# Kernel tuning notes

Hardware: AMD Instinct MI355X
Metric: run time of the kernel (lower is better)

## Reference

```python
import jax, jax.numpy as jnp
import numpy as np

TEMPERATURE = 1.0
B, H, S, D = 2, 16, 2048, 128

def setup_inputs() -> dict:
    key = jax.random.key(0)
    kq, kk, kv = jax.random.split(key, 3)
    q = jax.random.normal(kq, (B, H, S, D), dtype=jnp.float32)
    k = jax.random.normal(kk, (B, H, S, D), dtype=jnp.float32)
    v = jax.random.normal(kv, (B, H, S, D), dtype=jnp.float32)
    alpha = jnp.float32(0.5)  # nn.Parameter(torch.tensor(0.5))
    return {"q": q, "k": k, "v": v, "alpha": alpha}

def reference(q, k, v, alpha):
    # scores: [B,H,S,S]
    scores = jnp.einsum('bhqd,bhkd->bhqk', q, k) / TEMPERATURE
    row_mean = jnp.mean(scores, axis=-1, keepdims=True)  # [B,H,S,1]
    adaptive = alpha * scores + (1.0 - alpha) * row_mean
    attn = jax.nn.softmax(adaptive, axis=-1)
    return jnp.einsum('bhqk,bhkd->bhqd', attn, v)
```

## Files before the change

### kernel.cpp

```cpp
#include <hip/hip_runtime.h>


#define S_LEN 2048
#define HD    128
#define BQ    128
#define BK    64
#define NW    4
#define NT    (S_LEN / BK)
#define TILE_USH 16384

typedef __bf16    bf16x8 __attribute__((ext_vector_type(8)));
typedef __bf16    bf16x4 __attribute__((ext_vector_type(4)));
typedef _Float16  f16x8  __attribute__((ext_vector_type(8)));
typedef float     f32x4  __attribute__((ext_vector_type(4)));

__device__ __forceinline__ unsigned short f2bf(float x) {
  unsigned u = __builtin_bit_cast(unsigned, x);
  u = (u + 0x7FFFu + ((u >> 16) & 1u)) >> 16;
  return (unsigned short)u;
}
__device__ __forceinline__ unsigned short f2h(float x) {
  _Float16 h = (_Float16)x;
  return __builtin_bit_cast(unsigned short, h);
}
__device__ __forceinline__ float fast_exp2(float x) {
#if __has_builtin(__builtin_amdgcn_exp2f)
  return __builtin_amdgcn_exp2f(x);
#else
  return exp2f(x);
#endif
}

__global__ __launch_bounds__(256) void attn_prepass_kernel(
    const float* __restrict__ kg, const float* __restrict__ vg,
    unsigned short* __restrict__ ws) {
  const int blk  = blockIdx.x;
  const int head = blk >> 5;
  const int kt   = blk & 31;
  const int tid  = threadIdx.x;
  const size_t hoff = (size_t)head * S_LEN * HD;
  const float* kp = kg + hoff + (size_t)kt * BK * HD;
  const float* vp = vg + hoff + (size_t)kt * BK * HD;
  unsigned short* wsK  = ws + (size_t)blk * TILE_USH;
  unsigned short* wsVt = wsK + 8192;

#pragma unroll
  for (int it = 0; it < 4; ++it) {
    int idx = it * 256 + tid;
    int key = idx >> 4;
    int ch  = idx & 15;
    const float* src = kp + key * HD + ch * 8;
    float4 a = *(const float4*)src;
    float4 b = *(const float4*)(src + 4);
    float xs[8] = {a.x, a.y, a.z, a.w, b.x, b.y, b.z, b.w};
    union { unsigned short s[8]; uint4 v; } hi;
#pragma unroll
    for (int j = 0; j < 8; ++j) hi.s[j] = f2h(xs[j]);
    int slot = (ch & 8) | ((ch & 7) ^ (key & 7));
    *(uint4*)&wsK[key * 128 + slot * 8] = hi.v;
  }

#pragma unroll
  for (int it = 0; it < 4; ++it) {
    int idx = it * 256 + tid;
    int ch  = idx >> 7;
    int dim = idx & 127;
    union { unsigned short s[8]; uint4 v; } g;
#pragma unroll
    for (int j = 0; j < 8; ++j)
      g.s[j] = f2bf(vp[(size_t)(ch * 8 + j) * HD + dim]);
    int slot = ch ^ (dim & 7);
    *(uint4*)&wsVt[dim * 64 + slot * 8] = g.v;
  }
}

__device__ __forceinline__ void stage_tile(const unsigned short* __restrict__ wt,
                                           unsigned short* dst, int tid, int w) {
#pragma unroll
  for (int r = 0; r < 8; ++r) {
    const unsigned int* gp = (const unsigned int*)(wt + (size_t)(r * 256 + tid) * 8);
    unsigned short* lp = dst + (size_t)(r * 256 + w * 64) * 8;
    __builtin_amdgcn_global_load_lds(
        (const __attribute__((address_space(1))) unsigned int*)gp,
        (__attribute__((address_space(3))) unsigned int*)lp, 16, 0, 0);
  }
}

__global__ __launch_bounds__(256, 2) void adaptive_attn_kernel(
    const float* __restrict__ qg, const unsigned short* __restrict__ ws,
    const float* __restrict__ alphap, float* __restrict__ out) {
  __shared__ unsigned short sBuf[2][TILE_USH];
  __shared__ unsigned short sP[NW][2][1024];

  const int b    = blockIdx.x;
  const int head = (b & 7) * 4 + ((b >> 3) & 3);
  const int qt   = b >> 5;

  const int tid  = threadIdx.x;
  const int w    = tid >> 6;
  const int lane = tid & 63;
  const int g    = lane >> 4;
  const int qi   = lane & 15;

  const float lscale = alphap[0] * 1.44269504088896f;

  f16x8 qf[2][4];
#pragma unroll
  for (int h = 0; h < 2; ++h) {
    const int qrow = qt * BQ + w * 32 + h * 16 + qi;
    const float* qp = qg + (size_t)head * S_LEN * HD + (size_t)qrow * HD;
#pragma unroll
    for (int c = 0; c < 4; ++c) {
      float4 a  = *(const float4*)(qp + c * 32 + g * 8);
      float4 bb = *(const float4*)(qp + c * 32 + g * 8 + 4);
      float xs[8] = {a.x, a.y, a.z, a.w, bb.x, bb.y, bb.z, bb.w};
      union { f16x8 v; _Float16 s[8]; } hh;
#pragma unroll
      for (int j = 0; j < 8; ++j) hh.s[j] = (_Float16)(xs[j] * lscale);
      qf[h][c] = hh.v;
    }
  }

  f32x4 o[2][8];
#pragma unroll
  for (int h = 0; h < 2; ++h)
#pragma unroll
    for (int dt = 0; dt < 8; ++dt) o[h][dt] = (f32x4){0.f, 0.f, 0.f, 0.f};
  float lrun[2] = {0.f, 0.f};

  const unsigned short* wsh = ws + (size_t)head * NT * TILE_USH;

  stage_tile(wsh, &sBuf[0][0], tid, w);
  __syncthreads();

  for (int kt = 0; kt < NT; ++kt) {
    const unsigned short* sK  = &sBuf[kt & 1][0];
    const unsigned short* sVt = sK + 8192;

    if (kt + 1 < NT)
      stage_tile(wsh + (size_t)(kt + 1) * TILE_USH, &sBuf[(kt + 1) & 1][0], tid, w);

    f32x4 st[2][4];
#pragma unroll
    for (int mt = 0; mt < 4; ++mt) {
      f32x4 a0 = (f32x4){0.f, 0.f, 0.f, 0.f};
      f32x4 a1 = (f32x4){0.f, 0.f, 0.f, 0.f};
#pragma unroll
      for (int c = 0; c < 4; ++c) {
        int ch   = c * 4 + g;
        int slot = (ch & 8) | ((ch & 7) ^ (qi & 7));
        f16x8 ah = *(const f16x8*)&sK[(mt * 16 + qi) * 128 + slot * 8];
        a0 = __builtin_amdgcn_mfma_f32_16x16x32_f16(ah, qf[0][c], a0, 0, 0, 0);
        a1 = __builtin_amdgcn_mfma_f32_16x16x32_f16(ah, qf[1][c], a1, 0, 0, 0);
      }
      st[0][mt] = a0; st[1][mt] = a1;
    }

#pragma unroll
    for (int h = 0; h < 2; ++h) {
      unsigned short* sPh = &sP[w][h][0];
#pragma unroll
      for (int mt = 0; mt < 4; ++mt) {
        float p0 = fast_exp2(st[h][mt][0]);
        float p1 = fast_exp2(st[h][mt][1]);
        float p2 = fast_exp2(st[h][mt][2]);
        float p3 = fast_exp2(st[h][mt][3]);
        lrun[h] += (p0 + p1) + (p2 + p3);
        bf16x4 pv4;
        pv4[0] = (__bf16)p0; pv4[1] = (__bf16)p1;
        pv4[2] = (__bf16)p2; pv4[3] = (__bf16)p3;
        int slot = (mt * 2 + (g >> 1)) ^ (qi & 7);
        *(bf16x4*)&sPh[qi * 64 + slot * 8 + (g & 1) * 4] = pv4;
      }
    }

    bf16x8 pf[2][2];
#pragma unroll
    for (int h = 0; h < 2; ++h)
#pragma unroll
      for (int c = 0; c < 2; ++c) {
        int slot = (c * 4 + g) ^ (qi & 7);
        pf[h][c] = *(const bf16x8*)&sP[w][h][qi * 64 + slot * 8];
      }

#pragma unroll
    for (int dt = 0; dt < 8; ++dt) {
      f32x4 a0 = o[0][dt];
      f32x4 a1 = o[1][dt];
#pragma unroll
      for (int c = 0; c < 2; ++c) {
        int slot = (c * 4 + g) ^ (qi & 7);
        bf16x8 vf = *(const bf16x8*)&sVt[(dt * 16 + qi) * 64 + slot * 8];
        a0 = __builtin_amdgcn_mfma_f32_16x16x32_bf16(pf[0][c], vf, a0, 0, 0, 0);
        a1 = __builtin_amdgcn_mfma_f32_16x16x32_bf16(pf[1][c], vf, a1, 0, 0, 0);
      }
      o[0][dt] = a0; o[1][dt] = a1;
    }

    __syncthreads();
  }

  float* oph = out + (size_t)head * S_LEN * HD + (size_t)(qt * BQ + w * 32) * HD;
#pragma unroll
  for (int h = 0; h < 2; ++h) {
    float ltot = lrun[h];
    ltot += __shfl_xor(ltot, 16, 64);
    ltot += __shfl_xor(ltot, 32, 64);
    float inv[4];
#pragma unroll
    for (int r = 0; r < 4; ++r) {
      float lr = __shfl(ltot, g * 4 + r, 64);
      inv[r] = 1.0f / lr;
    }
    float* op = oph + (size_t)(h * 16) * HD;
#pragma unroll
    for (int dt = 0; dt < 8; ++dt) {
#pragma unroll
      for (int r = 0; r < 4; ++r) {
        op[(size_t)(g * 4 + r) * HD + dt * 16 + qi] = o[h][dt][r] * inv[r];
      }
    }
  }
}

extern "C" void kernel_launch(void* const* d_in, const int* in_sizes, int n_in,
                              void* d_out, int out_size, void* d_ws, size_t ws_size,
                              hipStream_t stream) {
  const float* q     = (const float*)d_in[0];
  const float* k     = (const float*)d_in[1];
  const float* v     = (const float*)d_in[2];
  const float* alpha = (const float*)d_in[3];
  float* out = (float*)d_out;
  unsigned short* ws = (unsigned short*)d_ws;

  hipLaunchKernelGGL(attn_prepass_kernel, dim3(1024), dim3(256), 0, stream,
                     k, v, ws);
  hipLaunchKernelGGL(adaptive_attn_kernel, dim3(512), dim3(256), 0, stream,
                     q, ws, alpha, out);
}
```

Before: 201.4 us.

## Software-pipeline PV MFMA one tile behind and transpose V via LDS

```diff
diff --git a/kernel.cpp b/kernel.cpp
--- a/kernel.cpp
+++ b/kernel.cpp
@@ -34,6 +34,7 @@
 __global__ __launch_bounds__(256) void attn_prepass_kernel(
     const float* __restrict__ kg, const float* __restrict__ vg,
     unsigned short* __restrict__ ws) {
+  __shared__ float T[64 * 130];
   const int blk  = blockIdx.x;
   const int head = blk >> 5;
   const int kt   = blk & 31;
@@ -61,16 +62,25 @@
   }
 
 #pragma unroll
-  for (int it = 0; it < 4; ++it) {
+  for (int it = 0; it < 16; ++it) {
     int idx = it * 256 + tid;
-    int ch  = idx >> 7;
-    int dim = idx & 127;
-    union { unsigned short s[8]; uint4 v; } g;
-#pragma unroll
-    for (int j = 0; j < 8; ++j)
-      g.s[j] = f2bf(vp[(size_t)(ch * 8 + j) * HD + dim]);
+    int key = idx >> 6;
+    int c2  = idx & 63;
+    float2 a = *(const float2*)(vp + (size_t)key * HD + c2 * 2);
+    *(float2*)&T[key * 130 + c2 * 2] = a;
+  }
+  __syncthreads();
+
+#pragma unroll
+  for (int r = 0; r < 4; ++r) {
+    int idx = r * 256 + tid;
+    int dim = idx >> 3;
+    int ch  = idx & 7;
+    union { unsigned short s[8]; uint4 v; } gg;
+#pragma unroll
+    for (int j = 0; j < 8; ++j) gg.s[j] = f2bf(T[(ch * 8 + j) * 130 + dim]);
     int slot = ch ^ (dim & 7);
-    *(uint4*)&wsVt[dim * 64 + slot * 8] = g.v;
+    *(uint4*)&wsVt[dim * 64 + slot * 8] = gg.v;
   }
 }
 
@@ -128,6 +138,9 @@
     for (int dt = 0; dt < 8; ++dt) o[h][dt] = (f32x4){0.f, 0.f, 0.f, 0.f};
   float lrun[2] = {0.f, 0.f};
 
+  bf16x8 vreg[8][2];
+  bf16x8 pf[2][2];
+
   const unsigned short* wsh = ws + (size_t)head * NT * TILE_USH;
 
   stage_tile(wsh, &sBuf[0][0], tid, w);
@@ -141,6 +154,7 @@
       stage_tile(wsh + (size_t)(kt + 1) * TILE_USH, &sBuf[(kt + 1) & 1][0], tid, w);
 
     f32x4 st[2][4];
+    __builtin_amdgcn_s_setprio(1);
 #pragma unroll
     for (int mt = 0; mt < 4; ++mt) {
       f32x4 a0 = (f32x4){0.f, 0.f, 0.f, 0.f};
@@ -154,6 +168,23 @@
         a1 = __builtin_amdgcn_mfma_f32_16x16x32_f16(ah, qf[1][c], a1, 0, 0, 0);
       }
       st[0][mt] = a0; st[1][mt] = a1;
+    }
+    __builtin_amdgcn_s_setprio(0);
+
+    if (kt > 0) {
+      __builtin_amdgcn_s_setprio(1);
+#pragma unroll
+      for (int dt = 0; dt < 8; ++dt) {
+        f32x4 a0 = o[0][dt];
+        f32x4 a1 = o[1][dt];
+#pragma unroll
+        for (int c = 0; c < 2; ++c) {
+          a0 = __builtin_amdgcn_mfma_f32_16x16x32_bf16(pf[0][c], vreg[dt][c], a0, 0, 0, 0);
+          a1 = __builtin_amdgcn_mfma_f32_16x16x32_bf16(pf[1][c], vreg[dt][c], a1, 0, 0, 0);
+        }
+        o[0][dt] = a0; o[1][dt] = a1;
+      }
+      __builtin_amdgcn_s_setprio(0);
     }
 
 #pragma unroll
@@ -174,7 +205,6 @@
       }
     }
 
-    bf16x8 pf[2][2];
 #pragma unroll
     for (int h = 0; h < 2; ++h)
 #pragma unroll
@@ -184,21 +214,29 @@
       }
 
 #pragma unroll
-    for (int dt = 0; dt < 8; ++dt) {
-      f32x4 a0 = o[0][dt];
-      f32x4 a1 = o[1][dt];
+    for (int dt = 0; dt < 8; ++dt)
 #pragma unroll
       for (int c = 0; c < 2; ++c) {
         int slot = (c * 4 + g) ^ (qi & 7);
-        bf16x8 vf = *(const bf16x8*)&sVt[(dt * 16 + qi) * 64 + slot * 8];
-        a0 = __builtin_amdgcn_mfma_f32_16x16x32_bf16(pf[0][c], vf, a0, 0, 0, 0);
-        a1 = __builtin_amdgcn_mfma_f32_16x16x32_bf16(pf[1][c], vf, a1, 0, 0, 0);
-      }
-      o[0][dt] = a0; o[1][dt] = a1;
-    }
+        vreg[dt][c] = *(const bf16x8*)&sVt[(dt * 16 + qi) * 64 + slot * 8];
+      }
 
     __syncthreads();
   }
+
+  __builtin_amdgcn_s_setprio(1);
+#pragma unroll
+  for (int dt = 0; dt < 8; ++dt) {
+    f32x4 a0 = o[0][dt];
+    f32x4 a1 = o[1][dt];
+#pragma unroll
+    for (int c = 0; c < 2; ++c) {
+      a0 = __builtin_amdgcn_mfma_f32_16x16x32_bf16(pf[0][c], vreg[dt][c], a0, 0, 0, 0);
+      a1 = __builtin_amdgcn_mfma_f32_16x16x32_bf16(pf[1][c], vreg[dt][c], a1, 0, 0, 0);
+    }
+    o[0][dt] = a0; o[1][dt] = a1;
+  }
+  __builtin_amdgcn_s_setprio(0);
 
   float* oph = out + (size_t)head * S_LEN * HD + (size_t)(qt * BQ + w * 32) * HD;
 #pragma unroll
```

Result: no change. 200.8 us (-0.3%).

## Use two waves with 64 query rows each and transpose V via LDS

Applied to the files above, without the earlier changes.

```diff
diff --git a/kernel.cpp b/kernel.cpp
--- a/kernel.cpp
+++ b/kernel.cpp
@@ -5,7 +5,8 @@
 #define HD    128
 #define BQ    128
 #define BK    64
-#define NW    4
+#define NW    2
+#define NH    4
 #define NT    (S_LEN / BK)
 #define TILE_USH 16384
 
@@ -34,6 +35,7 @@
 __global__ __launch_bounds__(256) void attn_prepass_kernel(
     const float* __restrict__ kg, const float* __restrict__ vg,
     unsigned short* __restrict__ ws) {
+  __shared__ float T[64 * 130];
   const int blk  = blockIdx.x;
   const int head = blk >> 5;
   const int kt   = blk & 31;
@@ -61,36 +63,45 @@
   }
 
 #pragma unroll
-  for (int it = 0; it < 4; ++it) {
+  for (int it = 0; it < 16; ++it) {
     int idx = it * 256 + tid;
-    int ch  = idx >> 7;
-    int dim = idx & 127;
-    union { unsigned short s[8]; uint4 v; } g;
-#pragma unroll
-    for (int j = 0; j < 8; ++j)
-      g.s[j] = f2bf(vp[(size_t)(ch * 8 + j) * HD + dim]);
+    int key = idx >> 6;
+    int c2  = idx & 63;
+    float2 a = *(const float2*)(vp + (size_t)key * HD + c2 * 2);
+    *(float2*)&T[key * 130 + c2 * 2] = a;
+  }
+  __syncthreads();
+
+#pragma unroll
+  for (int r = 0; r < 4; ++r) {
+    int idx = r * 256 + tid;
+    int dim = idx >> 3;
+    int ch  = idx & 7;
+    union { unsigned short s[8]; uint4 v; } gg;
+#pragma unroll
+    for (int j = 0; j < 8; ++j) gg.s[j] = f2bf(T[(ch * 8 + j) * 130 + dim]);
     int slot = ch ^ (dim & 7);
-    *(uint4*)&wsVt[dim * 64 + slot * 8] = g.v;
+    *(uint4*)&wsVt[dim * 64 + slot * 8] = gg.v;
   }
 }
 
 __device__ __forceinline__ void stage_tile(const unsigned short* __restrict__ wt,
                                            unsigned short* dst, int tid, int w) {
 #pragma unroll
-  for (int r = 0; r < 8; ++r) {
-    const unsigned int* gp = (const unsigned int*)(wt + (size_t)(r * 256 + tid) * 8);
-    unsigned short* lp = dst + (size_t)(r * 256 + w * 64) * 8;
+  for (int r = 0; r < 16; ++r) {
+    const unsigned int* gp = (const unsigned int*)(wt + (size_t)(r * 128 + tid) * 8);
+    unsigned short* lp = dst + (size_t)(r * 128 + w * 64) * 8;
     __builtin_amdgcn_global_load_lds(
         (const __attribute__((address_space(1))) unsigned int*)gp,
         (__attribute__((address_space(3))) unsigned int*)lp, 16, 0, 0);
   }
 }
 
-__global__ __launch_bounds__(256, 2) void adaptive_attn_kernel(
+__global__ __launch_bounds__(128, 1) void adaptive_attn_kernel(
     const float* __restrict__ qg, const unsigned short* __restrict__ ws,
     const float* __restrict__ alphap, float* __restrict__ out) {
   __shared__ unsigned short sBuf[2][TILE_USH];
-  __shared__ unsigned short sP[NW][2][1024];
+  __shared__ unsigned short sP[NW][NH][1024];
 
   const int b    = blockIdx.x;
   const int head = (b & 7) * 4 + ((b >> 3) & 3);
@@ -104,10 +115,10 @@
 
   const float lscale = alphap[0] * 1.44269504088896f;
 
-  f16x8 qf[2][4];
-#pragma unroll
-  for (int h = 0; h < 2; ++h) {
-    const int qrow = qt * BQ + w * 32 + h * 16 + qi;
+  f16x8 qf[NH][4];
+#pragma unroll
+  for (int h = 0; h < NH; ++h) {
+    const int qrow = qt * BQ + w * 64 + h * 16 + qi;
     const float* qp = qg + (size_t)head * S_LEN * HD + (size_t)qrow * HD;
 #pragma unroll
     for (int c = 0; c < 4; ++c) {
@@ -121,12 +132,12 @@
     }
   }
 
-  f32x4 o[2][8];
-#pragma unroll
-  for (int h = 0; h < 2; ++h)
+  f32x4 o[NH][8];
+#pragma unroll
+  for (int h = 0; h < NH; ++h)
 #pragma unroll
     for (int dt = 0; dt < 8; ++dt) o[h][dt] = (f32x4){0.f, 0.f, 0.f, 0.f};
-  float lrun[2] = {0.f, 0.f};
+  float lrun[NH] = {0.f, 0.f, 0.f, 0.f};
 
   const unsigned short* wsh = ws + (size_t)head * NT * TILE_USH;
 
@@ -140,43 +151,39 @@
     if (kt + 1 < NT)
       stage_tile(wsh + (size_t)(kt + 1) * TILE_USH, &sBuf[(kt + 1) & 1][0], tid, w);
 
-    f32x4 st[2][4];
 #pragma unroll
     for (int mt = 0; mt < 4; ++mt) {
-      f32x4 a0 = (f32x4){0.f, 0.f, 0.f, 0.f};
-      f32x4 a1 = (f32x4){0.f, 0.f, 0.f, 0.f};
+      f32x4 acc[NH];
+#pragma unroll
+      for (int h = 0; h < NH; ++h) acc[h] = (f32x4){0.f, 0.f, 0.f, 0.f};
 #pragma unroll
       for (int c = 0; c < 4; ++c) {
         int ch   = c * 4 + g;
         int slot = (ch & 8) | ((ch & 7) ^ (qi & 7));
         f16x8 ah = *(const f16x8*)&sK[(mt * 16 + qi) * 128 + slot * 8];
-        a0 = __builtin_amdgcn_mfma_f32_16x16x32_f16(ah, qf[0][c], a0, 0, 0, 0);
-        a1 = __builtin_amdgcn_mfma_f32_16x16x32_f16(ah, qf[1][c], a1, 0, 0, 0);
-      }
-      st[0][mt] = a0; st[1][mt] = a1;
-    }
-
-#pragma unroll
-    for (int h = 0; h < 2; ++h) {
-      unsigned short* sPh = &sP[w][h][0];
-#pragma unroll
-      for (int mt = 0; mt < 4; ++mt) {
-        float p0 = fast_exp2(st[h][mt][0]);
-        float p1 = fast_exp2(st[h][mt][1]);
-        float p2 = fast_exp2(st[h][mt][2]);
-        float p3 = fast_exp2(st[h][mt][3]);
+        acc[0] = __builtin_amdgcn_mfma_f32_16x16x32_f16(ah, qf[0][c], acc[0], 0, 0, 0);
+        acc[1] = __builtin_amdgcn_mfma_f32_16x16x32_f16(ah, qf[1][c], acc[1], 0, 0, 0);
+        acc[2] = __builtin_amdgcn_mfma_f32_16x16x32_f16(ah, qf[2][c], acc[2], 0, 0, 0);
+        acc[3] = __builtin_amdgcn_mfma_f32_16x16x32_f16(ah, qf[3][c], acc[3], 0, 0, 0);
+      }
+#pragma unroll
+      for (int h = 0; h < NH; ++h) {
+        float p0 = fast_exp2(acc[h][0]);
+        float p1 = fast_exp2(acc[h][1]);
+        float p2 = fast_exp2(acc[h][2]);
+        float p3 = fast_exp2(acc[h][3]);
         lrun[h] += (p0 + p1) + (p2 + p3);
         bf16x4 pv4;
         pv4[0] = (__bf16)p0; pv4[1] = (__bf16)p1;
         pv4[2] = (__bf16)p2; pv4[3] = (__bf16)p3;
         int slot = (mt * 2 + (g >> 1)) ^ (qi & 7);
-        *(bf16x4*)&sPh[qi * 64 + slot * 8 + (g & 1) * 4] = pv4;
-      }
-    }
-
-    bf16x8 pf[2][2];
-#pragma unroll
-    for (int h = 0; h < 2; ++h)
+        *(bf16x4*)&sP[w][h][qi * 64 + slot * 8 + (g & 1) * 4] = pv4;
+      }
+    }
+
+    bf16x8 pf[NH][2];
+#pragma unroll
+    for (int h = 0; h < NH; ++h)
 #pragma unroll
       for (int c = 0; c < 2; ++c) {
         int slot = (c * 4 + g) ^ (qi & 7);
@@ -185,24 +192,23 @@
 
 #pragma unroll
     for (int dt = 0; dt < 8; ++dt) {
-      f32x4 a0 = o[0][dt];
-      f32x4 a1 = o[1][dt];
 #pragma unroll
       for (int c = 0; c < 2; ++c) {
         int slot = (c * 4 + g) ^ (qi & 7);
         bf16x8 vf = *(const bf16x8*)&sVt[(dt * 16 + qi) * 64 + slot * 8];
-        a0 = __builtin_amdgcn_mfma_f32_16x16x32_bf16(pf[0][c], vf, a0, 0, 0, 0);
-        a1 = __builtin_amdgcn_mfma_f32_16x16x32_bf16(pf[1][c], vf, a1, 0, 0, 0);
-      }
-      o[0][dt] = a0; o[1][dt] = a1;
+        o[0][dt] = __builtin_amdgcn_mfma_f32_16x16x32_bf16(pf[0][c], vf, o[0][dt], 0, 0, 0);
+        o[1][dt] = __builtin_amdgcn_mfma_f32_16x16x32_bf16(pf[1][c], vf, o[1][dt], 0, 0, 0);
+        o[2][dt] = __builtin_amdgcn_mfma_f32_16x16x32_bf16(pf[2][c], vf, o[2][dt], 0, 0, 0);
+        o[3][dt] = __builtin_amdgcn_mfma_f32_16x16x32_bf16(pf[3][c], vf, o[3][dt], 0, 0, 0);
+      }
     }
 
     __syncthreads();
   }
 
-  float* oph = out + (size_t)head * S_LEN * HD + (size_t)(qt * BQ + w * 32) * HD;
-#pragma unroll
-  for (int h = 0; h < 2; ++h) {
+  float* oph = out + (size_t)head * S_LEN * HD + (size_t)(qt * BQ + w * 64) * HD;
+#pragma unroll
+  for (int h = 0; h < NH; ++h) {
     float ltot = lrun[h];
     ltot += __shfl_xor(ltot, 16, 64);
     ltot += __shfl_xor(ltot, 32, 64);
@@ -235,6 +241,6 @@
 
   hipLaunchKernelGGL(attn_prepass_kernel, dim3(1024), dim3(256), 0, stream,
                      k, v, ws);
-  hipLaunchKernelGGL(adaptive_attn_kernel, dim3(512), dim3(256), 0, stream,
+  hipLaunchKernelGGL(adaptive_attn_kernel, dim3(512), dim3(128), 0, stream,
                      q, ws, alpha, out);
 }
```

Result: slower. 228.1 us (+13.2%).
